# Performance work log

Measured on AMD Instinct MI355X. Metric: run time of the kernel, lower is better.

Reference implementation:

```python
import jax, jax.numpy as jnp
import numpy as np


def setup_inputs() -> dict:
    key = jax.random.key(0)
    kc, kh, kx, kwx, kwh = jax.random.split(key, 5)
    B, T, D, H = 64, 512, 1024, 1024
    c0 = jax.random.normal(kc, (B, H), dtype=jnp.float32)
    h0 = jax.random.normal(kh, (B, H), dtype=jnp.float32)
    xs = jax.random.normal(kx, (B, T, D), dtype=jnp.float32)
    # fan-in scaled init like lecun_normal (flax default)
    Wx = jax.random.normal(kwx, (D, 4 * H), dtype=jnp.float32) / np.sqrt(D)
    Wh = jax.random.normal(kwh, (H, 4 * H), dtype=jnp.float32) / np.sqrt(H)
    b = jnp.zeros((4 * H,), dtype=jnp.float32)
    return {"c0": c0, "h0": h0, "xs": xs, "Wx": Wx, "Wh": Wh, "b": b}


def _lstm(c0, h0, xs, Wx, Wh, b):
    # Batch the input-to-hidden projection across all timesteps (compute-dense GEMM)
    xproj = jnp.einsum('btd,dh->tbh', xs, Wx)  # [T, B, 4H], time-major for scan

    def step(carry, xp):
        c, h = carry
        gates = xp + h @ Wh + b                # [B, 4H]
        i, f, g, o = jnp.split(gates, 4, axis=-1)  # flax gate order: i, f, g, o
        new_c = jax.nn.sigmoid(f) * c + jax.nn.sigmoid(i) * jnp.tanh(g)
        new_h = jax.nn.sigmoid(o) * jnp.tanh(new_c)
        return (new_c, new_h), new_h

    (cT, hT), ys = jax.lax.scan(step, (c0, h0), xproj)
    return (cT, hT), jnp.transpose(ys, (1, 0, 2))  # ys back to [B, T, H]


def reference(c0, h0, xs, Wx, Wh, b):
    return _lstm(c0, h0, xs, Wx, Wh, b)
```

## Files before the change

### kernel.cpp

```cpp
#include <hip/hip_runtime.h>


typedef _Float16 half8 __attribute__((ext_vector_type(8)));
typedef float floatx4 __attribute__((ext_vector_type(4)));

__device__ __forceinline__ void gll16(const void* g, void* l) {
  __builtin_amdgcn_global_load_lds(
      (const __attribute__((address_space(1))) unsigned int*)g,
      (__attribute__((address_space(3))) unsigned int*)l, 16, 0, 0);
}

__device__ __forceinline__ float sigm(float x) { return 1.f / (1.f + __expf(-x)); }
__device__ __forceinline__ float tanhfast(float x) { return 1.f - 2.f / (__expf(2.f * x) + 1.f); }

__global__ void prep_ew(const float* __restrict__ xs, const float* __restrict__ h0,
                        _Float16* __restrict__ xs16, _Float16* __restrict__ hb0,
                        int* __restrict__ flags) {
  long gid = (long)blockIdx.x * blockDim.x + threadIdx.x;
  if (gid < 4194304) {
    const float4* p = (const float4*)xs + gid * 2;
    float4 u = p[0], w = p[1];
    half8 o;
    o[0] = (_Float16)u.x; o[1] = (_Float16)u.y; o[2] = (_Float16)u.z; o[3] = (_Float16)u.w;
    o[4] = (_Float16)w.x; o[5] = (_Float16)w.y; o[6] = (_Float16)w.z; o[7] = (_Float16)w.w;
    long e = gid * 8;
    long row = e >> 10;
    long b = row >> 9, t = row & 511;
    *(half8*)(xs16 + ((t << 6) + b) * 1024 + (e & 1023)) = o;
  } else if (gid < 4202496) {
    long j = gid - 4194304;
    const float4* p = (const float4*)h0 + j * 2;
    float4 u = p[0], w = p[1];
    half8 o;
    o[0] = (_Float16)u.x; o[1] = (_Float16)u.y; o[2] = (_Float16)u.z; o[3] = (_Float16)u.w;
    o[4] = (_Float16)w.x; o[5] = (_Float16)w.y; o[6] = (_Float16)w.z; o[7] = (_Float16)w.w;
    *(half8*)(hb0 + j * 8) = o;
  } else if (gid < 4203264) {
    flags[gid - 4202496] = 0;
  }
}

__global__ void transpose_k(const float* __restrict__ in, _Float16* __restrict__ outp) {
  __shared__ float s[32][33];
  int bx = blockIdx.x * 32, by = blockIdx.y * 32;
  int tx = threadIdx.x, ty = threadIdx.y;
#pragma unroll
  for (int k = 0; k < 32; k += 8)
    s[ty + k][tx] = in[(long)(by + ty + k) * 4096 + bx + tx];
  __syncthreads();
#pragma unroll
  for (int k = 0; k < 32; k += 8)
    outp[(long)(bx + ty + k) * 1024 + by + tx] = (_Float16)s[tx][ty + k];
}

__global__ __launch_bounds__(256, 1) void fused(const _Float16* __restrict__ xs16,
                                                const _Float16* __restrict__ wxt,
                                                _Float16* __restrict__ xprj,
                                                const _Float16* __restrict__ wht,
                                                const float* __restrict__ bias,
                                                const float* __restrict__ c0,
                                                _Float16* __restrict__ hbuf,
                                                int* __restrict__ flags,
                                                float* __restrict__ out) {
  __shared__ char smem[131072];
  const int tid = threadIdx.x;
  int* const cnt = flags + 256;
  int* const tot = flags + 512;

  if (blockIdx.x >= 64) {
    _Float16* sA = (_Float16*)smem;
    _Float16* sB = (_Float16*)(smem + 8192);
    const int gid = blockIdx.x - 64;
    const int by = gid >> 5, bx = gid & 31;

    {
      int it = 0;
      for (;;) {
        int tp = __hip_atomic_load(&flags[0], __ATOMIC_RELAXED, __HIP_MEMORY_SCOPE_AGENT);
        if (tp >= 2 * by - 48 || ++it > 256) break;
        __builtin_amdgcn_s_sleep(64);
      }
    }

    const int w = tid >> 6, l = tid & 63, li = l & 15, q = l >> 4;
    const int wr = w >> 1, wc = w & 1;
    const int m0 = by * 128, n0 = bx * 128;
    floatx4 acc[4][4] = {};
    const _Float16* gA0 = xs16 + (long)(m0 + (w * 16 + li)) * 1024 + q * 8;
    const _Float16* gA1 = xs16 + (long)(m0 + ((4 + w) * 16 + li)) * 1024 + q * 8;
    const _Float16* gB0 = wxt + (long)(n0 + (w * 16 + li)) * 1024 + q * 8;
    const _Float16* gB1 = wxt + (long)(n0 + ((4 + w) * 16 + li)) * 1024 + q * 8;
    _Float16* lA0 = sA + (w * 64) * 8;
    _Float16* lA1 = sA + (256 + w * 64) * 8;
    _Float16* lB0 = sB + (w * 64) * 8;
    _Float16* lB1 = sB + (256 + w * 64) * 8;
    for (int k0 = 0; k0 < 1024; k0 += 32) {
      __syncthreads();
      gll16(gA0 + k0, lA0);
      gll16(gA1 + k0, lA1);
      gll16(gB0 + k0, lB0);
      gll16(gB1 + k0, lB1);
      __syncthreads();
      half8 af[4], bf[4];
      const half8* pA = (const half8*)sA;
      const half8* pB = (const half8*)sB;
#pragma unroll
      for (int i = 0; i < 4; i++) af[i] = pA[(wr * 4 + i) * 64 + l];
#pragma unroll
      for (int j = 0; j < 4; j++) bf[j] = pB[(wc * 4 + j) * 64 + l];
#pragma unroll
      for (int i = 0; i < 4; i++)
#pragma unroll
        for (int j = 0; j < 4; j++)
          acc[i][j] = __builtin_amdgcn_mfma_f32_16x16x32_f16(af[i], bf[j], acc[i][j], 0, 0, 0);
    }
#pragma unroll
    for (int i = 0; i < 4; i++) {
#pragma unroll
      for (int r = 0; r < 4; r++) {
        int m = m0 + wr * 64 + i * 16 + q * 4 + r;
#pragma unroll
        for (int j = 0; j < 4; j++) {
          int gn = n0 + wc * 64 + j * 16 + li;
          xprj[(long)m * 4096 + gn] = (_Float16)acc[i][j][r];
        }
      }
    }
    __syncthreads();
    if (tid == 0) {
      __builtin_amdgcn_fence(__ATOMIC_RELEASE, "agent");
      __hip_atomic_fetch_add(&cnt[by], 1, __ATOMIC_RELAXED, __HIP_MEMORY_SCOPE_AGENT);
      __hip_atomic_fetch_add(tot, 1, __ATOMIC_RELAXED, __HIP_MEMORY_SCOPE_AGENT);
    }
    return;
  }

  _Float16* sW = (_Float16*)smem;
  const int wgid = blockIdx.x;
  const int v = tid >> 6;
  const int l = tid & 63, li = l & 15, q = l >> 4;
  const int ks = wgid * 16;

#pragma unroll 4
  for (int i = 0; i < 32; i++) {
    int c = i * 256 + tid;
    int g = c >> 11, kk = (c >> 6) & 31;
    int cli = c & 15, cq = (c >> 4) & 3;
    gll16(wht + (long)((g << 10) + ks + cli) * 1024 + kk * 32 + cq * 8,
          sW + (long)(c - l) * 8);
  }
  float creg[4];
#pragma unroll
  for (int r = 0; r < 4; r++)
    creg[r] = c0[(long)(v * 16 + q * 4 + r) * 1024 + ks + li];
  float bs[4];
#pragma unroll
  for (int g = 0; g < 4; g++) bs[g] = bias[(g << 10) + ks + li];
  __syncthreads();

  const half8* pW = (const half8*)sW;
  const int fidx = 4 * l + v;
  int xdone = 0;

  for (int t = 0; t < 512; t++) {
    if (!xdone && !(t & 1)) {
      const int nb = t >> 1;
      for (;;) {
        int cr = __hip_atomic_load(&cnt[nb], __ATOMIC_RELAXED, __HIP_MEMORY_SCOPE_AGENT);
        if (cr >= 32) break;
        __builtin_amdgcn_s_sleep(16);
      }
      xdone = (__hip_atomic_load(tot, __ATOMIC_RELAXED, __HIP_MEMORY_SCOPE_AGENT) >= 8192);
      __builtin_amdgcn_fence(__ATOMIC_ACQUIRE, "agent");
    }

    const _Float16* xpt = xprj + (long)t * 262144 + ks + li;
    _Float16 xv[4][4];
#pragma unroll
    for (int g = 0; g < 4; g++)
#pragma unroll
      for (int r = 0; r < 4; r++)
        xv[g][r] = xpt[(long)(v * 16 + q * 4 + r) * 4096 + (g << 10)];

    for (;;) {
      int f = __hip_atomic_load(&flags[fidx], __ATOMIC_RELAXED, __HIP_MEMORY_SCOPE_AGENT);
      if (__all(f >= t)) break;
      __builtin_amdgcn_s_sleep(1);
    }
    __builtin_amdgcn_fence(__ATOMIC_ACQUIRE, "workgroup");

    const _Float16* hrow = hbuf + (long)t * 65536 + (long)(v * 16 + li) * 1024 + q * 8;
    floatx4 acc[4] = {};
    half8 ap[8];
#pragma unroll
    for (int p = 0; p < 8; p++) ap[p] = *(const half8*)(hrow + p * 32);
#pragma unroll
    for (int kk = 0; kk < 32; kk++) {
      half8 a = ap[kk & 7];
#pragma unroll
      for (int g = 0; g < 4; g++)
        acc[g] = __builtin_amdgcn_mfma_f32_16x16x32_f16(a, pW[((g * 32 + kk) << 6) + l], acc[g], 0, 0, 0);
      if (kk < 24) ap[kk & 7] = *(const half8*)(hrow + (kk + 8) * 32);
    }

    _Float16* hnext = hbuf + (long)(t + 1) * 65536;
    float hval[4], cval[4];
#pragma unroll
    for (int r = 0; r < 4; r++) {
      float gi = acc[0][r] + (float)xv[0][r] + bs[0];
      float gf = acc[1][r] + (float)xv[1][r] + bs[1];
      float gg = acc[2][r] + (float)xv[2][r] + bs[2];
      float go = acc[3][r] + (float)xv[3][r] + bs[3];
      float cN = sigm(gf) * creg[r] + sigm(gi) * tanhfast(gg);
      creg[r] = cN;
      cval[r] = cN;
      float hN = sigm(go) * tanhfast(cN);
      hval[r] = hN;
      int b = v * 16 + q * 4 + r;
      unsigned short hu = __builtin_bit_cast(unsigned short, (_Float16)hN);
      __hip_atomic_store((unsigned short*)hnext + (long)b * 1024 + ks + li, hu,
                         __ATOMIC_RELAXED, __HIP_MEMORY_SCOPE_AGENT);
    }
    __builtin_amdgcn_s_waitcnt(0);
    if (l == 0)
      __hip_atomic_store(&flags[4 * wgid + v], t + 1, __ATOMIC_RELAXED, __HIP_MEMORY_SCOPE_AGENT);

#pragma unroll
    for (int r = 0; r < 4; r++) {
      int b = v * 16 + q * 4 + r;
      out[131072 + (long)b * 524288 + (long)t * 1024 + ks + li] = hval[r];
      if (t == 511) {
        out[(long)b * 1024 + ks + li] = cval[r];
        out[65536 + (long)b * 1024 + ks + li] = hval[r];
      }
    }
  }
}

extern "C" void kernel_launch(void* const* d_in, const int* in_sizes, int n_in,
                              void* d_out, int out_size, void* d_ws, size_t ws_size,
                              hipStream_t stream) {
  const float* c0 = (const float*)d_in[0];
  const float* h0 = (const float*)d_in[1];
  const float* xs = (const float*)d_in[2];
  const float* Wx = (const float*)d_in[3];
  const float* Wh = (const float*)d_in[4];
  const float* bias = (const float*)d_in[5];
  float* out = (float*)d_out;

  char* ws = (char*)d_ws;
  size_t off = 0;
  _Float16* xs16 = (_Float16*)(ws + off); off += 67108864;
  _Float16* wxt  = (_Float16*)(ws + off); off += 8388608;
  _Float16* wht  = (_Float16*)(ws + off); off += 8388608;
  _Float16* xprj = (_Float16*)(ws + off); off += 268435456;
  _Float16* hbuf = (_Float16*)(ws + off); off += 67239936;
  int* flags     = (int*)(ws + off);      off += 4096;
  if (ws_size < off) return;

  prep_ew<<<16419, 256, 0, stream>>>(xs, h0, xs16, hbuf, flags);
  transpose_k<<<dim3(128, 32), dim3(32, 8), 0, stream>>>(Wx, wxt);
  transpose_k<<<dim3(128, 32), dim3(32, 8), 0, stream>>>(Wh, wht);
  fused<<<8256, 256, 0, stream>>>(xs16, wxt, xprj, wht, bias, c0, hbuf, flags, out);
}
```

Baseline: 5.795 ms.

## Store input projection in per-workgroup blocked layout for vectorized recurrent loads

```diff
diff --git a/kernel.cpp b/kernel.cpp
--- a/kernel.cpp
+++ b/kernel.cpp
@@ -2,6 +2,7 @@
 
 
 typedef _Float16 half8 __attribute__((ext_vector_type(8)));
+typedef _Float16 half4 __attribute__((ext_vector_type(4)));
 typedef float floatx4 __attribute__((ext_vector_type(4)));
 
 __device__ __forceinline__ void gll16(const void* g, void* l) {
@@ -114,15 +115,21 @@
         for (int j = 0; j < 4; j++)
           acc[i][j] = __builtin_amdgcn_mfma_f32_16x16x32_f16(af[i], bf[j], acc[i][j], 0, 0, 0);
     }
-#pragma unroll
-    for (int i = 0; i < 4; i++) {
-#pragma unroll
-      for (int r = 0; r < 4; r++) {
-        int m = m0 + wr * 64 + i * 16 + q * 4 + r;
+    {
+      const int t_ = by * 2 + wr;
+#pragma unroll
+      for (int i = 0; i < 4; i++) {
 #pragma unroll
         for (int j = 0; j < 4; j++) {
-          int gn = n0 + wc * 64 + j * 16 + li;
-          xprj[(long)m * 4096 + gn] = (_Float16)acc[i][j][r];
+          int n_ = n0 + wc * 64 + j * 16;
+          int g_ = n_ >> 10, wg_ = (n_ & 1023) >> 4;
+          half4 hv;
+          hv[0] = (_Float16)acc[i][j][0];
+          hv[1] = (_Float16)acc[i][j][1];
+          hv[2] = (_Float16)acc[i][j][2];
+          hv[3] = (_Float16)acc[i][j][3];
+          *(half4*)(xprj + ((long)(t_ * 64 + wg_)) * 4096 +
+                    (long)((i * 4 + q) * 16 + li) * 16 + g_ * 4) = hv;
         }
       }
     }
@@ -174,13 +181,9 @@
       __builtin_amdgcn_fence(__ATOMIC_ACQUIRE, "agent");
     }
 
-    const _Float16* xpt = xprj + (long)t * 262144 + ks + li;
-    _Float16 xv[4][4];
-#pragma unroll
-    for (int g = 0; g < 4; g++)
-#pragma unroll
-      for (int r = 0; r < 4; r++)
-        xv[g][r] = xpt[(long)(v * 16 + q * 4 + r) * 4096 + (g << 10)];
+    const _Float16* xpt = xprj + ((long)t * 64 + wgid) * 4096 + (long)(v * 64 + l) * 16;
+    half8 xv0 = *(const half8*)(xpt);
+    half8 xv1 = *(const half8*)(xpt + 8);
 
     for (;;) {
       int f = __hip_atomic_load(&flags[fidx], __ATOMIC_RELAXED, __HIP_MEMORY_SCOPE_AGENT);
@@ -207,10 +210,10 @@
     float hval[4], cval[4];
 #pragma unroll
     for (int r = 0; r < 4; r++) {
-      float gi = acc[0][r] + (float)xv[0][r] + bs[0];
-      float gf = acc[1][r] + (float)xv[1][r] + bs[1];
-      float gg = acc[2][r] + (float)xv[2][r] + bs[2];
-      float go = acc[3][r] + (float)xv[3][r] + bs[3];
+      float gi = acc[0][r] + (float)xv0[r] + bs[0];
+      float gf = acc[1][r] + (float)xv0[4 + r] + bs[1];
+      float gg = acc[2][r] + (float)xv1[r] + bs[2];
+      float go = acc[3][r] + (float)xv1[4 + r] + bs[3];
       float cN = sigm(gf) * creg[r] + sigm(gi) * tanhfast(gg);
       creg[r] = cN;
       cval[r] = cN;
```

Result: no change. 5.909 ms (+2.0%).
